# Kernel optimization log

Measured on AMD Instinct MI355X. Metric: run time of the kernel, lower is better.

The kernel has to match this reference:

```python
import jax, jax.numpy as jnp
import numpy as np

N_NODES = 50000
N_EDGES = 800000
N_GRAPHS = 512
H = 64
F_NODE = 32
F_EDGE = 8
N_CLASSES = 10
EPS = 1e-5


def _bn(x, w, b):
    # BatchNorm1d in training mode: batch stats, biased variance
    m = jnp.mean(x, axis=0)
    v = jnp.mean(jnp.square(x - m), axis=0)
    return (x - m) * jax.lax.rsqrt(v + EPS) * w + b


def setup_inputs() -> dict:
    key = jax.random.key(0)
    ks = jax.random.split(key, 12)
    s = 0.02
    inp = {
        "x": jax.random.normal(ks[0], (N_NODES, F_NODE), jnp.float32),
        "edge_attr": jax.random.normal(ks[1], (N_EDGES, F_EDGE), jnp.float32),
        "edge_index": jax.random.randint(ks[2], (2, N_EDGES), 0, N_NODES),
        "batch": jnp.sort(jax.random.randint(ks[3], (N_NODES,), 0, N_GRAPHS)),
        "bn_feat_w": jnp.ones((F_NODE,), jnp.float32),
        "bn_feat_b": jnp.full((F_NODE,), 1e-4, jnp.float32),
        "Wn0": jax.random.normal(ks[4], (F_NODE, H), jnp.float32) * s,
        "bn0": jnp.zeros((H,), jnp.float32),
        "We0": jax.random.normal(ks[5], (2 * H + F_EDGE, H), jnp.float32) * s,
        "be0": jnp.zeros((H,), jnp.float32),
        "bns_w": jnp.ones((3, H), jnp.float32),
        "bns_b": jnp.full((3, H), 1e-4, jnp.float32),
        "Wn": jax.random.normal(ks[6], (3, H, H), jnp.float32) * s,
        "Wnb": jnp.zeros((3, H), jnp.float32),
        "We": jax.random.normal(ks[7], (3, 3 * H, H), jnp.float32) * s,
        "Web": jnp.zeros((3, H), jnp.float32),
        "bn_fc_w": jnp.ones((H,), jnp.float32),
        "bn_fc_b": jnp.full((H,), 1e-4, jnp.float32),
        "Wfc": jax.random.normal(ks[8], (H, H), jnp.float32) * s,
        "bfc": jnp.zeros((H,), jnp.float32),
        "bn_hid_w": jnp.ones((H,), jnp.float32),
        "bn_hid_b": jnp.full((H,), 1e-4, jnp.float32),
        "Wcls": jax.random.normal(ks[9], (H, N_CLASSES), jnp.float32) * s,
        "bcls": jnp.zeros((N_CLASSES,), jnp.float32),
    }
    return inp


def reference(x, edge_attr, edge_index, batch, bn_feat_w, bn_feat_b, Wn0, bn0,
              We0, be0, bns_w, bns_b, Wn, Wnb, We, Web, bn_fc_w, bn_fc_b,
              Wfc, bfc, bn_hid_w, bn_hid_b, Wcls, bcls):
    src, dst = edge_index[0], edge_index[1]
    n = x.shape[0]
    # symmetric GCN edge normalization (edge_norm=True)
    deg = jax.ops.segment_sum(jnp.ones_like(src, jnp.float32), dst, num_segments=n)
    dinv = jax.lax.rsqrt(jnp.maximum(deg, 1.0))
    norm = (dinv[src] * dinv[dst])[:, None]  # [E,1]

    # feature conv (gfn=True: linear transforms only, no propagation)
    h = _bn(x, bn_feat_w, bn_feat_b) @ Wn0 + bn0  # [N,H]
    e = (h[src] @ We0[:H] + h[dst] @ We0[H:2 * H]
         + edge_attr @ We0[2 * H:] + be0)         # [E,H]
    h = jax.nn.relu(h)
    e = jax.nn.relu(e)

    # stacked edge-gated GCN convs: BN -> conv(gather/scatter) -> ReLU
    for i in range(3):
        ht = _bn(h, bns_w[i], bns_b[i]) @ Wn[i] + Wnb[i]          # [N,H]
        hs = ht[src]                                               # [E,H] gather
        ei = (hs @ We[i, :H] + ht[dst] @ We[i, H:2 * H]
              + e @ We[i, 2 * H:] + Web[i])                        # [E,H]
        msg = norm * hs * jax.nn.sigmoid(ei)                       # edge-gated message
        h = jax.nn.relu(jax.ops.segment_sum(msg, dst, num_segments=n))

    # global_add_pool over graphs
    g = jax.ops.segment_sum(h, batch, num_segments=N_GRAPHS)       # [G,H]
    g = jax.nn.relu(_bn(g, bn_fc_w, bn_fc_b) @ Wfc + bfc)
    g = _bn(g, bn_hid_w, bn_hid_b) @ Wcls + bcls
    return jax.nn.log_softmax(g, axis=-1)
```

## Files before the change

kernel.cpp:

```cpp
#include <hip/hip_runtime.h>
#include <hip/hip_bf16.h>

#define N_NODESC 50000
#define N_EDGESC 800000
#define N_GRAPHSC 512
#define HDIM 64
#define FNODE 32
#define FEDGE 8
#define NCLS 10
#define BN_EPS 1e-5f
#define SCAN_B 256
#define SCAN_G 196
#define NPW 8

typedef __bf16 bf16x8 __attribute__((ext_vector_type(8)));
typedef float f32x4 __attribute__((ext_vector_type(4)));
typedef unsigned int uint32;

static __device__ __forceinline__ float bcast(float v, int k) {
  return __uint_as_float(__builtin_amdgcn_readlane(__float_as_uint(v), k));
}
static __device__ __forceinline__ int bcast_i(int v, int k) {
  return __builtin_amdgcn_readlane(v, k);
}
static __device__ __forceinline__ unsigned short f2bu(float f) {
  __hip_bfloat16 b = __float2bfloat16(f);
  return *reinterpret_cast<unsigned short*>(&b);
}
static __device__ __forceinline__ float bu2f(unsigned short u) {
  __hip_bfloat16 b;
  *reinterpret_cast<unsigned short*>(&b) = u;
  return __bfloat162float(b);
}

__global__ void k_deg(const int* __restrict__ dst, uint32* __restrict__ degi) {
  int e = blockIdx.x * blockDim.x + threadIdx.x;
  if (e < N_EDGESC) atomicAdd(&degi[dst[e]], 1u);
}

__global__ void k_scan1(const uint32* __restrict__ degi, uint32* __restrict__ ptr,
                        uint32* __restrict__ bsum, float* __restrict__ dinv) {
  __shared__ uint32 s[SCAN_B];
  int t = threadIdx.x;
  int i = blockIdx.x * SCAN_B + t;
  uint32 v = (i < N_NODESC) ? degi[i] : 0u;
  if (i < N_NODESC) dinv[i] = rsqrtf(fmaxf((float)v, 1.0f));
  s[t] = v; __syncthreads();
  for (int off = 1; off < SCAN_B; off <<= 1) {
    uint32 x = (t >= off) ? s[t - off] : 0u; __syncthreads();
    s[t] += x; __syncthreads();
  }
  if (i < N_NODESC) ptr[i] = s[t] - v;
  if (t == SCAN_B - 1) bsum[blockIdx.x] = s[t];
}

__global__ void k_scan2(uint32* __restrict__ bsum) {
  __shared__ uint32 s[256];
  int t = threadIdx.x;
  uint32 v = (t < SCAN_G) ? bsum[t] : 0u;
  s[t] = v; __syncthreads();
  for (int off = 1; off < 256; off <<= 1) {
    uint32 x = (t >= off) ? s[t - off] : 0u; __syncthreads();
    s[t] += x; __syncthreads();
  }
  if (t < SCAN_G) bsum[t] = s[t] - v;
}

__global__ void k_scan3(uint32* __restrict__ ptr, const uint32* __restrict__ bsum) {
  int i = blockIdx.x * SCAN_B + threadIdx.x;
  if (i < N_NODESC) ptr[i] += bsum[blockIdx.x];
  if (blockIdx.x == 0 && threadIdx.x == 0) ptr[N_NODESC] = N_EDGESC;
}

template <int C>
__global__ void k_colstats(const float* __restrict__ in, int nrows, float* __restrict__ stats) {
  const int RPB = 256 / C;
  int tid = threadIdx.x;
  int col = tid % C;
  int rowOff = tid / C;
  float s = 0.f, s2 = 0.f;
  for (int r = blockIdx.x * RPB + rowOff; r < nrows; r += gridDim.x * RPB) {
    float v = in[r * C + col];
    s += v; s2 += v * v;
  }
  __shared__ float ls[256], ls2[256];
  ls[tid] = s; ls2[tid] = s2;
  __syncthreads();
  for (int off = 128; off >= C; off >>= 1) {
    if (tid < off) { ls[tid] += ls[tid + off]; ls2[tid] += ls2[tid + off]; }
    __syncthreads();
  }
  if (tid < C) {
    atomicAdd(&stats[tid], ls[tid]);
    atomicAdd(&stats[C + tid], ls2[tid]);
  }
}

template <int CIN, int COUT>
__global__ void k_foldbn(const float* __restrict__ stats, float invN,
                         const float* __restrict__ bnw, const float* __restrict__ bnb,
                         const float* __restrict__ W, const float* __restrict__ bias,
                         float* __restrict__ Wf, float* __restrict__ bf) {
  __shared__ float a[CIN], sh[CIN];
  int tid = threadIdx.x;
  if (tid < CIN) {
    float m = stats[tid] * invN;
    float v = stats[CIN + tid] * invN - m * m;
    float inv = rsqrtf(v + BN_EPS);
    float aa = bnw[tid] * inv;
    a[tid] = aa;
    sh[tid] = bnb[tid] - m * aa;
  }
  __syncthreads();
  for (int i = tid; i < CIN * COUT; i += 256) {
    int r = i / COUT;
    Wf[i] = a[r] * W[i];
  }
  if (tid < COUT) {
    float acc = bias ? bias[tid] : 0.f;
    for (int r = 0; r < CIN; ++r) acc += sh[r] * W[r * COUT + tid];
    bf[tid] = acc;
  }
}

template <int K, bool RELU>
__global__ void k_nodemm(const float* __restrict__ in, int nrows,
                         const float* __restrict__ W, const float* __restrict__ bias,
                         float* __restrict__ out) {
  int tid = threadIdx.x;
  int lane = tid & 63;
  float w[K];
#pragma unroll
  for (int k = 0; k < K; ++k) w[k] = W[k * 64 + lane];
  float bv = bias ? bias[lane] : 0.f;
  int wave = (blockIdx.x * blockDim.x + tid) >> 6;
  int nwaves = (gridDim.x * blockDim.x) >> 6;
  for (int r = wave; r < nrows; r += nwaves) {
    float rv = (lane < K) ? in[(size_t)r * K + lane] : 0.f;
    float acc = bv;
#pragma unroll
    for (int k = 0; k < K; ++k) acc = fmaf(bcast(rv, k), w[k], acc);
    if (RELU) acc = fmaxf(acc, 0.f);
    out[(size_t)r * 64 + lane] = acc;
  }
}

__global__ void __launch_bounds__(256, 2) k_stage0(
    const float* __restrict__ x, int nrows,
    const float* __restrict__ Wf, const float* __restrict__ bfv,
    const float* __restrict__ WA, const float* __restrict__ bA,
    const float* __restrict__ WB,
    float* __restrict__ h, unsigned short* __restrict__ hAb,
    unsigned short* __restrict__ hBb) {
  int tid = threadIdx.x;
  int lane = tid & 63;
  float w0[FNODE], wA[64], wB[64];
#pragma unroll
  for (int k = 0; k < FNODE; ++k) w0[k] = Wf[k * 64 + lane];
#pragma unroll
  for (int k = 0; k < 64; ++k) wA[k] = WA[k * 64 + lane];
#pragma unroll
  for (int k = 0; k < 64; ++k) wB[k] = WB[k * 64 + lane];
  float b0 = bfv[lane];
  float b2 = bA[lane];
  int wave = (blockIdx.x * blockDim.x + tid) >> 6;
  int nwaves = (gridDim.x * blockDim.x) >> 6;
  for (int r = wave; r < nrows; r += nwaves) {
    float xv = (lane < FNODE) ? x[(size_t)r * FNODE + lane] : 0.f;
    float t0 = b0;
#pragma unroll
    for (int k = 0; k < FNODE; ++k) t0 = fmaf(bcast(xv, k), w0[k], t0);
    float aA = b2, aB = 0.f;
#pragma unroll
    for (int k = 0; k < 64; ++k) {
      float tb = bcast(t0, k);
      aA = fmaf(tb, wA[k], aA);
      aB = fmaf(tb, wB[k], aB);
    }
    h[(size_t)r * 64 + lane] = fmaxf(t0, 0.f);
    hAb[(size_t)r * 64 + lane] = f2bu(aA);
    hBb[(size_t)r * 64 + lane] = f2bu(aB);
  }
}

__global__ void __launch_bounds__(256, 2) k_node3(
    const float* __restrict__ h, int nrows,
    const float* __restrict__ stats, float invN,
    const float* __restrict__ bnw, const float* __restrict__ bnb,
    const float* __restrict__ Wn_i, const float* __restrict__ Wnb_i,
    const float* __restrict__ WA, const float* __restrict__ Wab,
    const float* __restrict__ WB,
    uint32* __restrict__ htP, unsigned short* __restrict__ htBb) {
  __shared__ float a_s[64], sh_s[64];
  int tid = threadIdx.x;
  int lane = tid & 63;
  if (tid < 64) {
    float m = stats[tid] * invN;
    float v = stats[64 + tid] * invN - m * m;
    float inv = rsqrtf(v + BN_EPS);
    float aa = bnw[tid] * inv;
    a_s[tid] = aa;
    sh_s[tid] = bnb[tid] - m * aa;
  }
  __syncthreads();
  float w1[64], w2[64], w3[64];
  float b1 = Wnb_i[lane];
#pragma unroll
  for (int k = 0; k < 64; ++k) {
    float raw = Wn_i[k * 64 + lane];
    w1[k] = a_s[k] * raw;
    b1 = fmaf(sh_s[k], raw, b1);
  }
#pragma unroll
  for (int k = 0; k < 64; ++k) w2[k] = WA[k * 64 + lane];
#pragma unroll
  for (int k = 0; k < 64; ++k) w3[k] = WB[k * 64 + lane];
  float b2 = Wab[lane];
  int cperm = (lane & 15) * 4 + (lane >> 4);
  int wave = (blockIdx.x * blockDim.x + tid) >> 6;
  int nwaves = (gridDim.x * blockDim.x) >> 6;
  for (int r = wave; r < nrows; r += nwaves) {
    float hv = h[(size_t)r * 64 + lane];
    float t1 = b1;
#pragma unroll
    for (int k = 0; k < 64; ++k) t1 = fmaf(bcast(hv, k), w1[k], t1);
    float t2 = b2;
    float t3 = 0.f;
#pragma unroll
    for (int k = 0; k < 64; ++k) {
      float tb = bcast(t1, k);
      t2 = fmaf(tb, w2[k], t2);
      t3 = fmaf(tb, w3[k], t3);
    }
    htP[(size_t)r * 64 + cperm] = ((uint32)f2bu(t2) << 16) | (uint32)f2bu(t1);
    htBb[(size_t)r * 64 + lane] = f2bu(t3);
  }
}

__global__ void k_scatedge(
    const int* __restrict__ src, const int* __restrict__ dst,
    const float* __restrict__ ea, const float* __restrict__ dinv,
    const uint32* __restrict__ ptr, uint32* __restrict__ cursor,
    const unsigned short* __restrict__ hAb, const unsigned short* __restrict__ hBb,
    const float* __restrict__ Wc,
    int* __restrict__ srcs, int* __restrict__ dsts, float* __restrict__ normf,
    __hip_bfloat16* __restrict__ ebf) {
  int tid = threadIdx.x;
  int lane = tid & 63;
  float w[FEDGE];
#pragma unroll
  for (int k = 0; k < FEDGE; ++k) w[k] = Wc[k * 64 + lane];
  int wave = (blockIdx.x * blockDim.x + tid) >> 6;
  int nwaves = (gridDim.x * blockDim.x) >> 6;
  const int nquads = N_EDGESC / 4;
  int per = (nquads + nwaves - 1) / nwaves;
  int p0 = wave * per;
  int p1 = min(p0 + per, nquads);
  for (int pr = p0; pr < p1; ++pr) {
    int e = 4 * pr;
    int sv = (lane < 4) ? src[e + lane] : 0;
    int dv = (lane < 4) ? dst[e + lane] : 0;
    int s_j[4], d_j[4];
#pragma unroll
    for (int j = 0; j < 4; ++j) { s_j[j] = bcast_i(sv, j); d_j[j] = bcast_i(dv, j); }
    uint32 idx_l = 0;
    if (lane < 4) {
      uint32 rk = atomicAdd(&cursor[dv], 1u);
      idx_l = ptr[dv] + rk;
      srcs[idx_l] = sv;
      dsts[idx_l] = dv;
      normf[idx_l] = dinv[sv] * dinv[dv];
    }
    int i_j[4];
#pragma unroll
    for (int j = 0; j < 4; ++j) i_j[j] = bcast_i((int)idx_l, j);
    float eav = (lane < 32) ? ea[(size_t)e * FEDGE + lane] : 0.f;
    unsigned short a0 = hAb[(size_t)s_j[0] * 64 + lane], b0 = hBb[(size_t)d_j[0] * 64 + lane];
    unsigned short a1 = hAb[(size_t)s_j[1] * 64 + lane], b1 = hBb[(size_t)d_j[1] * 64 + lane];
    unsigned short a2 = hAb[(size_t)s_j[2] * 64 + lane], b2 = hBb[(size_t)d_j[2] * 64 + lane];
    unsigned short a3 = hAb[(size_t)s_j[3] * 64 + lane], b3 = hBb[(size_t)d_j[3] * 64 + lane];
    float acc0 = bu2f(a0) + bu2f(b0);
    float acc1 = bu2f(a1) + bu2f(b1);
    float acc2 = bu2f(a2) + bu2f(b2);
    float acc3 = bu2f(a3) + bu2f(b3);
#pragma unroll
    for (int k = 0; k < FEDGE; ++k) {
      acc0 = fmaf(bcast(eav, 0 * 8 + k), w[k], acc0);
      acc1 = fmaf(bcast(eav, 1 * 8 + k), w[k], acc1);
      acc2 = fmaf(bcast(eav, 2 * 8 + k), w[k], acc2);
      acc3 = fmaf(bcast(eav, 3 * 8 + k), w[k], acc3);
    }
    unsigned short* ob = reinterpret_cast<unsigned short*>(ebf);
    __builtin_nontemporal_store(f2bu(fmaxf(acc0, 0.f)), ob + (size_t)i_j[0] * 64 + lane);
    __builtin_nontemporal_store(f2bu(fmaxf(acc1, 0.f)), ob + (size_t)i_j[1] * 64 + lane);
    __builtin_nontemporal_store(f2bu(fmaxf(acc2, 0.f)), ob + (size_t)i_j[2] * 64 + lane);
    __builtin_nontemporal_store(f2bu(fmaxf(acc3, 0.f)), ob + (size_t)i_j[3] * 64 + lane);
  }
}

__global__ void __launch_bounds__(256, 4) k_conv_mfma(
    const __hip_bfloat16* __restrict__ ebf,
    const float* __restrict__ We2,
    const uint32* __restrict__ htP, const unsigned short* __restrict__ htBb,
    const float* __restrict__ normf,
    const int* __restrict__ srcs, const int* __restrict__ dsts,
    const uint32* __restrict__ ptr,
    float* __restrict__ hout, float* __restrict__ stats,
    const int* __restrict__ batch, float* __restrict__ gout) {
  __shared__ float lds_acc[4][NPW * 65];
  __shared__ float lds_htB[4][NPW * 65];
  __shared__ float st_s[64], st_s2[64];
  const int tid = threadIdx.x;
  const int lane = tid & 63;
  const int w = tid >> 6;
  const int m = lane & 15;
  const int kg = lane >> 4;

  int wave = blockIdx.x * 4 + w;
  int n0 = wave * NPW;
  bool validw = (n0 < N_NODESC);

  if (stats) {
    if (tid < 64) { st_s[tid] = 0.f; st_s2[tid] = 0.f; }
    __syncthreads();
  }

  bf16x8 b[4][2];
#pragma unroll
  for (int t = 0; t < 4; ++t)
#pragma unroll
    for (int s = 0; s < 2; ++s)
#pragma unroll
      for (int j = 0; j < 8; ++j) {
        int k = s * 32 + kg * 8 + j;
        int c = t * 16 + m;
        b[t][s][j] = (__bf16)We2[k * 64 + c];
      }

  float* acc_l = lds_acc[w];
  float* htB_l = lds_htB[w];
#pragma unroll
  for (int r = 0; r < NPW; ++r) {
    acc_l[r * 65 + lane] = 0.f;
    htB_l[r * 65 + lane] = validw ? bu2f(htBb[(size_t)(n0 + r) * 64 + lane]) : 0.f;
  }

  int e0 = validw ? (int)ptr[n0] : 0;
  int eend = validw ? (int)ptr[n0 + NPW] : 0;
  int tb0 = e0 & ~15;

  float run[4] = {0.f, 0.f, 0.f, 0.f};
  int dcur = -1, rcur = 0;

  for (int tb = tb0; tb < eend; tb += 16) {
    const bf16x8* arow = reinterpret_cast<const bf16x8*>(ebf + (size_t)(tb + m) * 64 + kg * 8);
    bf16x8 a0 = __builtin_nontemporal_load(arow);
    bf16x8 a1 = __builtin_nontemporal_load(arow + 4);
    int rb = tb + kg * 4;
    int4 sev = *reinterpret_cast<const int4*>(srcs + rb);
    int4 dev = *reinterpret_cast<const int4*>(dsts + rb);
    float4 nev = *reinterpret_cast<const float4*>(normf + rb);
    int se[4] = {sev.x, sev.y, sev.z, sev.w};
    int de[4] = {dev.x, dev.y, dev.z, dev.w};
    float ne[4] = {nev.x, nev.y, nev.z, nev.w};
    uint4 pv[4];
#pragma unroll
    for (int j = 0; j < 4; ++j)
      pv[j] = *reinterpret_cast<const uint4*>(htP + (size_t)se[j] * 64 + m * 4);

    f32x4 acc[4];
#pragma unroll
    for (int t = 0; t < 4; ++t) {
      f32x4 z = {0.f, 0.f, 0.f, 0.f};
      acc[t] = __builtin_amdgcn_mfma_f32_16x16x32_bf16(a0, b[t][0], z, 0, 0, 0);
      acc[t] = __builtin_amdgcn_mfma_f32_16x16x32_bf16(a1, b[t][1], acc[t], 0, 0, 0);
    }

#pragma unroll
    for (int j = 0; j < 4; ++j) {
      int eidx = rb + j;
      bool valid = (eidx >= e0) && (eidx < eend);
      if (valid) {
        if (de[j] != dcur) {
          if (dcur >= 0) {
#pragma unroll
            for (int t = 0; t < 4; ++t) {
              atomicAdd(&acc_l[rcur * 65 + t * 16 + m], run[t]);
              run[t] = 0.f;
            }
          }
          dcur = de[j];
          rcur = dcur - n0;
        }
        uint32 pd[4] = {pv[j].x, pv[j].y, pv[j].z, pv[j].w};
#pragma unroll
        for (int t = 0; t < 4; ++t) {
          int c = t * 16 + m;
          float gate = acc[t][j] + bu2f((unsigned short)(pd[t] >> 16)) + htB_l[rcur * 65 + c];
          float sig = 1.0f / (1.0f + __expf(-gate));
          run[t] = fmaf(ne[j] * bu2f((unsigned short)(pd[t] & 0xffffu)), sig, run[t]);
        }
      }
    }
  }
  if (dcur >= 0) {
#pragma unroll
    for (int t = 0; t < 4; ++t)
      atomicAdd(&acc_l[rcur * 65 + t * 16 + m], run[t]);
  }

  if (gout) {
    if (validw) {
      int bcur = batch[n0];
      float racc = 0.f;
#pragma unroll
      for (int r = 0; r < NPW; ++r) {
        float v = fmaxf(acc_l[r * 65 + lane], 0.f);
        int bb = batch[n0 + r];
        if (bb != bcur) {
          atomicAdd(&gout[(size_t)bcur * 64 + lane], racc);
          racc = 0.f;
          bcur = bb;
        }
        racc += v;
      }
      atomicAdd(&gout[(size_t)bcur * 64 + lane], racc);
    }
  } else {
    float s = 0.f, s2 = 0.f;
    if (validw) {
#pragma unroll
      for (int r = 0; r < NPW; ++r) {
        float v = fmaxf(acc_l[r * 65 + lane], 0.f);
        hout[(size_t)(n0 + r) * 64 + lane] = v;
        s += v; s2 += v * v;
      }
    }
    if (stats) {
      atomicAdd(&st_s[lane], s);
      atomicAdd(&st_s2[lane], s2);
      __syncthreads();
      if (tid < 64) atomicAdd(&stats[tid], st_s[tid]);
      else if (tid < 128) atomicAdd(&stats[tid], st_s2[tid - 64]);
    }
  }
}

__global__ void k_cls(const float* __restrict__ g2, const float* __restrict__ Wc,
                      const float* __restrict__ bc, float* __restrict__ out) {
  int r = blockIdx.x * blockDim.x + threadIdx.x;
  if (r >= N_GRAPHSC) return;
  float z[NCLS];
#pragma unroll
  for (int c = 0; c < NCLS; ++c) z[c] = bc[c];
  for (int k = 0; k < HDIM; ++k) {
    float v = g2[r * HDIM + k];
#pragma unroll
    for (int c = 0; c < NCLS; ++c) z[c] = fmaf(v, Wc[k * NCLS + c], z[c]);
  }
  float m = z[0];
#pragma unroll
  for (int c = 1; c < NCLS; ++c) m = fmaxf(m, z[c]);
  float ssum = 0.f;
#pragma unroll
  for (int c = 0; c < NCLS; ++c) ssum += __expf(z[c] - m);
  float l = __logf(ssum);
#pragma unroll
  for (int c = 0; c < NCLS; ++c) out[r * NCLS + c] = z[c] - m - l;
}

extern "C" void kernel_launch(void* const* d_in, const int* in_sizes, int n_in,
                              void* d_out, int out_size, void* d_ws, size_t ws_size,
                              hipStream_t stream) {
  const float* x         = (const float*)d_in[0];
  const float* edge_attr = (const float*)d_in[1];
  const int*   ei        = (const int*)d_in[2];
  const int*   batch     = (const int*)d_in[3];
  const float* bn_feat_w = (const float*)d_in[4];
  const float* bn_feat_b = (const float*)d_in[5];
  const float* Wn0       = (const float*)d_in[6];
  const float* bn0       = (const float*)d_in[7];
  const float* We0       = (const float*)d_in[8];
  const float* be0       = (const float*)d_in[9];
  const float* bns_w     = (const float*)d_in[10];
  const float* bns_b     = (const float*)d_in[11];
  const float* Wn        = (const float*)d_in[12];
  const float* Wnb       = (const float*)d_in[13];
  const float* We        = (const float*)d_in[14];
  const float* Web       = (const float*)d_in[15];
  const float* bn_fc_w   = (const float*)d_in[16];
  const float* bn_fc_b   = (const float*)d_in[17];
  const float* Wfc       = (const float*)d_in[18];
  const float* bfc       = (const float*)d_in[19];
  const float* bn_hid_w  = (const float*)d_in[20];
  const float* bn_hid_b  = (const float*)d_in[21];
  const float* Wcls      = (const float*)d_in[22];
  const float* bcls      = (const float*)d_in[23];
  float* out = (float*)d_out;
  const int* src = ei;
  const int* dst = ei + N_EDGESC;

  char* p = (char*)d_ws;
  auto carve = [&](size_t bytes) {
    char* q = p;
    p += (bytes + 255) & ~(size_t)255;
    return q;
  };
  __hip_bfloat16* ebf = (__hip_bfloat16*)carve((size_t)N_EDGESC * 64 * 2);
  float* h    = (float*)carve((size_t)N_NODESC * 64 * 4);
  uint32* htP = (uint32*)carve((size_t)N_NODESC * 64 * 4);
  unsigned short* htBb = (unsigned short*)carve((size_t)N_NODESC * 64 * 2);
  unsigned short* hAb  = (unsigned short*)carve((size_t)N_NODESC * 64 * 2);
  unsigned short* hBb  = (unsigned short*)carve((size_t)N_NODESC * 64 * 2);
  float* dinv = (float*)carve((size_t)N_NODESC * 4);
  float* g    = (float*)carve((size_t)N_GRAPHSC * 64 * 4);
  float* g2   = (float*)carve((size_t)N_GRAPHSC * 64 * 4);
  float* stats= (float*)carve(6 * 128 * 4);
  float* Wf   = (float*)carve(64 * 64 * 4);
  float* bf   = (float*)carve(64 * 4);
  uint32* degi   = (uint32*)carve((size_t)50176 * 4);
  uint32* ptr    = (uint32*)carve((size_t)50176 * 4);
  uint32* cursor = (uint32*)carve((size_t)50176 * 4);
  uint32* bsum   = (uint32*)carve(256 * 4);
  int* srcs  = (int*)carve((size_t)N_EDGESC * 4);
  int* dsts  = (int*)carve((size_t)N_EDGESC * 4);
  float* normf = (float*)carve((size_t)N_EDGESC * 4);

  float* st_x  = stats;
  float* st_h0 = stats + 128;
  float* st_h1 = stats + 256;
  float* st_h2 = stats + 384;
  float* st_g  = stats + 512;
  float* st_g2 = stats + 640;

  hipMemsetAsync(degi, 0, (size_t)3 * 50176 * 4, stream);
  hipMemsetAsync(stats, 0, 6 * 128 * 4, stream);
  hipMemsetAsync(g, 0, N_GRAPHSC * 64 * 4, stream);

  k_deg<<<(N_EDGESC + 255) / 256, 256, 0, stream>>>(dst, degi);
  k_scan1<<<SCAN_G, SCAN_B, 0, stream>>>(degi, ptr, bsum, dinv);
  k_scan2<<<1, 256, 0, stream>>>(bsum);
  k_scan3<<<SCAN_G, SCAN_B, 0, stream>>>(ptr, bsum);

  k_colstats<FNODE><<<256, 256, 0, stream>>>(x, N_NODESC, st_x);
  k_foldbn<FNODE, HDIM><<<1, 256, 0, stream>>>(st_x, 1.f / N_NODESC, bn_feat_w, bn_feat_b, Wn0, bn0, Wf, bf);
  k_stage0<<<512, 256, 0, stream>>>(x, N_NODESC, Wf, bf, We0, be0, We0 + 64 * 64, h, hAb, hBb);

  k_scatedge<<<1024, 256, 0, stream>>>(src, dst, edge_attr, dinv, ptr, cursor,
                                       hAb, hBb, We0 + 128 * 64, srcs, dsts, normf, ebf);
  k_colstats<HDIM><<<256, 256, 0, stream>>>(h, N_NODESC, st_h0);

  const int convBlocks = (N_NODESC / NPW + 3) / 4;
  float* inSlot[3]  = {st_h0, st_h1, st_h2};
  float* outSlot[3] = {st_h1, st_h2, nullptr};
  for (int i = 0; i < 3; ++i) {
    const float* WeI = We + (size_t)i * 192 * 64;
    k_node3<<<512, 256, 0, stream>>>(h, N_NODESC, inSlot[i], 1.f / N_NODESC,
                                     bns_w + i * 64, bns_b + i * 64,
                                     Wn + (size_t)i * 64 * 64, Wnb + i * 64,
                                     WeI, Web + i * 64, WeI + 64 * 64, htP, htBb);
    k_conv_mfma<<<convBlocks, 256, 0, stream>>>(ebf, WeI + 128 * 64, htP, htBb, normf,
                                                srcs, dsts, ptr, h, outSlot[i],
                                                batch, (i == 2) ? g : nullptr);
  }

  k_colstats<HDIM><<<32, 256, 0, stream>>>(g, N_GRAPHSC, st_g);
  k_foldbn<HDIM, HDIM><<<1, 256, 0, stream>>>(st_g, 1.f / N_GRAPHSC, bn_fc_w, bn_fc_b, Wfc, bfc, Wf, bf);
  k_nodemm<HDIM, true><<<128, 256, 0, stream>>>(g, N_GRAPHSC, Wf, bf, g2);
  k_colstats<HDIM><<<32, 256, 0, stream>>>(g2, N_GRAPHSC, st_g2);
  k_foldbn<HDIM, NCLS><<<1, 256, 0, stream>>>(st_g2, 1.f / N_GRAPHSC, bn_hid_w, bn_hid_b, Wcls, bcls, Wf, bf);
  k_cls<<<(N_GRAPHSC + 255) / 256, 256, 0, stream>>>(g2, Wf, bf, out);
}
```

Measured before the change: 679.8 us.

## Pack per-edge src/dst/norm into 16-byte records and fuse h0 stats into stage0

Replaces the three separate CSR-sorted edge arrays (srcs, dsts, normf) with one interleaved int4 record per edge. The scatter kernel writes each record with a single nontemporal 16-byte store instead of three scattered 4-byte stores, and the conv kernel reads four records per lane group. Column statistics for the first hidden layer are now accumulated inside k_stage0 through LDS and global atomics, which drops a separate colstats pass over h. The cost is 33% more edge-metadata bytes (an unused padding word) and a change in the conv load pattern from three vector loads to four.

```diff
diff --git a/kernel.cpp b/kernel.cpp
--- a/kernel.cpp
+++ b/kernel.cpp
@@ -15,6 +15,7 @@
 
 typedef __bf16 bf16x8 __attribute__((ext_vector_type(8)));
 typedef float f32x4 __attribute__((ext_vector_type(4)));
+typedef int i32x4 __attribute__((ext_vector_type(4)));
 typedef unsigned int uint32;
 
 static __device__ __forceinline__ float bcast(float v, int k) {
@@ -151,9 +152,12 @@
     const float* __restrict__ WA, const float* __restrict__ bA,
     const float* __restrict__ WB,
     float* __restrict__ h, unsigned short* __restrict__ hAb,
-    unsigned short* __restrict__ hBb) {
+    unsigned short* __restrict__ hBb, float* __restrict__ stats) {
+  __shared__ float st_s[64], st_s2[64];
   int tid = threadIdx.x;
   int lane = tid & 63;
+  if (tid < 64) { st_s[tid] = 0.f; st_s2[tid] = 0.f; }
+  __syncthreads();
   float w0[FNODE], wA[64], wB[64];
 #pragma unroll
   for (int k = 0; k < FNODE; ++k) w0[k] = Wf[k * 64 + lane];
@@ -165,6 +169,7 @@
   float b2 = bA[lane];
   int wave = (blockIdx.x * blockDim.x + tid) >> 6;
   int nwaves = (gridDim.x * blockDim.x) >> 6;
+  float s = 0.f, s2 = 0.f;
   for (int r = wave; r < nrows; r += nwaves) {
     float xv = (lane < FNODE) ? x[(size_t)r * FNODE + lane] : 0.f;
     float t0 = b0;
@@ -177,10 +182,17 @@
       aA = fmaf(tb, wA[k], aA);
       aB = fmaf(tb, wB[k], aB);
     }
-    h[(size_t)r * 64 + lane] = fmaxf(t0, 0.f);
+    float hv = fmaxf(t0, 0.f);
+    h[(size_t)r * 64 + lane] = hv;
+    s += hv; s2 += hv * hv;
     hAb[(size_t)r * 64 + lane] = f2bu(aA);
     hBb[(size_t)r * 64 + lane] = f2bu(aB);
   }
+  atomicAdd(&st_s[lane], s);
+  atomicAdd(&st_s2[lane], s2);
+  __syncthreads();
+  if (tid < 64) atomicAdd(&stats[tid], st_s[tid]);
+  else if (tid < 128) atomicAdd(&stats[tid], st_s2[tid - 64]);
 }
 
 __global__ void __launch_bounds__(256, 2) k_node3(
@@ -243,7 +255,7 @@
     const uint32* __restrict__ ptr, uint32* __restrict__ cursor,
     const unsigned short* __restrict__ hAb, const unsigned short* __restrict__ hBb,
     const float* __restrict__ Wc,
-    int* __restrict__ srcs, int* __restrict__ dsts, float* __restrict__ normf,
+    int* __restrict__ edge4,
     __hip_bfloat16* __restrict__ ebf) {
   int tid = threadIdx.x;
   int lane = tid & 63;
@@ -267,9 +279,11 @@
     if (lane < 4) {
       uint32 rk = atomicAdd(&cursor[dv], 1u);
       idx_l = ptr[dv] + rk;
-      srcs[idx_l] = sv;
-      dsts[idx_l] = dv;
-      normf[idx_l] = dinv[sv] * dinv[dv];
+      i32x4 q;
+      q.x = sv; q.y = dv;
+      q.z = __float_as_int(dinv[sv] * dinv[dv]);
+      q.w = 0;
+      __builtin_nontemporal_store(q, reinterpret_cast<i32x4*>(edge4) + idx_l);
     }
     int i_j[4];
 #pragma unroll
@@ -302,8 +316,7 @@
     const __hip_bfloat16* __restrict__ ebf,
     const float* __restrict__ We2,
     const uint32* __restrict__ htP, const unsigned short* __restrict__ htBb,
-    const float* __restrict__ normf,
-    const int* __restrict__ srcs, const int* __restrict__ dsts,
+    const int* __restrict__ edge4,
     const uint32* __restrict__ ptr,
     float* __restrict__ hout, float* __restrict__ stats,
     const int* __restrict__ batch, float* __restrict__ gout) {
@@ -357,12 +370,13 @@
     bf16x8 a0 = __builtin_nontemporal_load(arow);
     bf16x8 a1 = __builtin_nontemporal_load(arow + 4);
     int rb = tb + kg * 4;
-    int4 sev = *reinterpret_cast<const int4*>(srcs + rb);
-    int4 dev = *reinterpret_cast<const int4*>(dsts + rb);
-    float4 nev = *reinterpret_cast<const float4*>(normf + rb);
-    int se[4] = {sev.x, sev.y, sev.z, sev.w};
-    int de[4] = {dev.x, dev.y, dev.z, dev.w};
-    float ne[4] = {nev.x, nev.y, nev.z, nev.w};
+    int se[4], de[4];
+    float ne[4];
+#pragma unroll
+    for (int j = 0; j < 4; ++j) {
+      i32x4 q = *reinterpret_cast<const i32x4*>(edge4 + (size_t)(rb + j) * 4);
+      se[j] = q.x; de[j] = q.y; ne[j] = __int_as_float(q.z);
+    }
     uint4 pv[4];
 #pragma unroll
     for (int j = 0; j < 4; ++j)
@@ -522,9 +536,7 @@
   uint32* ptr    = (uint32*)carve((size_t)50176 * 4);
   uint32* cursor = (uint32*)carve((size_t)50176 * 4);
   uint32* bsum   = (uint32*)carve(256 * 4);
-  int* srcs  = (int*)carve((size_t)N_EDGESC * 4);
-  int* dsts  = (int*)carve((size_t)N_EDGESC * 4);
-  float* normf = (float*)carve((size_t)N_EDGESC * 4);
+  int* edge4 = (int*)carve((size_t)N_EDGESC * 4 * 4);
 
   float* st_x  = stats;
   float* st_h0 = stats + 128;
@@ -544,11 +556,10 @@
 
   k_colstats<FNODE><<<256, 256, 0, stream>>>(x, N_NODESC, st_x);
   k_foldbn<FNODE, HDIM><<<1, 256, 0, stream>>>(st_x, 1.f / N_NODESC, bn_feat_w, bn_feat_b, Wn0, bn0, Wf, bf);
-  k_stage0<<<512, 256, 0, stream>>>(x, N_NODESC, Wf, bf, We0, be0, We0 + 64 * 64, h, hAb, hBb);
+  k_stage0<<<512, 256, 0, stream>>>(x, N_NODESC, Wf, bf, We0, be0, We0 + 64 * 64, h, hAb, hBb, st_h0);
 
   k_scatedge<<<1024, 256, 0, stream>>>(src, dst, edge_attr, dinv, ptr, cursor,
-                                       hAb, hBb, We0 + 128 * 64, srcs, dsts, normf, ebf);
-  k_colstats<HDIM><<<256, 256, 0, stream>>>(h, N_NODESC, st_h0);
+                                       hAb, hBb, We0 + 128 * 64, edge4, ebf);
 
   const int convBlocks = (N_NODESC / NPW + 3) / 4;
   float* inSlot[3]  = {st_h0, st_h1, st_h2};
@@ -559,8 +570,8 @@
                                      bns_w + i * 64, bns_b + i * 64,
                                      Wn + (size_t)i * 64 * 64, Wnb + i * 64,
                                      WeI, Web + i * 64, WeI + 64 * 64, htP, htBb);
-    k_conv_mfma<<<convBlocks, 256, 0, stream>>>(ebf, WeI + 128 * 64, htP, htBb, normf,
-                                                srcs, dsts, ptr, h, outSlot[i],
+    k_conv_mfma<<<convBlocks, 256, 0, stream>>>(ebf, WeI + 128 * 64, htP, htBb, edge4,
+                                                ptr, h, outSlot[i],
                                                 batch, (i == 2) ? g : nullptr);
   }
 
```

Measured after the change: 682.0 us. No clear change (+0.3%).
